# Performance work log

Hardware: AMD Instinct MI355X
Metric: run time of the kernel (lower is better)

Reference implementation:

```python
import jax, jax.numpy as jnp
import numpy as np

LARGE = 1.0e6  # sentinel distance for 'no feature pixel found'
ALPHA, GAMMA = 0.25, 2.0
SMOOTH, LAMBDA = 1e-06, 1.0


def _col_dist(feat):
    # feat: [B,H,W] bool. Distance along axis 1 to nearest True at-or-before each row.
    H = feat.shape[1]
    i = jnp.arange(H, dtype=jnp.float32)[None, :, None]
    pos = jnp.where(feat, i, -LARGE)
    return i - jax.lax.cummax(pos, axis=1)


def _edt(feat):
    # Exact Euclidean distance transform: distance from every pixel to nearest True pixel.
    # Pass 1: 1-D distance along axis 1 (two directional scans via cummax).
    g = jnp.minimum(_col_dist(feat), jnp.flip(_col_dist(jnp.flip(feat, 1)), 1))
    g = jnp.minimum(g, LARGE)  # columns with no feature
    # Pass 2: d^2(i,j) = min_k g(i,k)^2 + (j-k)^2  (exact separable EDT)
    W = feat.shape[2]
    j = jnp.arange(W, dtype=jnp.float32)
    cost = (j[:, None] - j[None, :]) ** 2  # [W(j), W(k)]
    d2 = jnp.min(g[:, :, None, :] ** 2 + cost[None, None, :, :], axis=-1)  # [B,H,W]
    return jnp.sqrt(d2)


def _distance_weights(targets_f):
    # targets_f: [B,1,H,W] float 0/1 -> beta weights [B,1,H,W]
    m = targets_f[:, 0]  # [B,H,W]
    fg = _edt(m <= 0.5)  # dist of fg pixels to nearest bg (0 on bg) == scipy edt(m>0.5)
    bg = _edt(m > 0.5)   # dist of bg pixels to nearest fg (0 on fg) == scipy edt(m<=0.5)
    dist = jnp.where(m > 0.5, fg, -bg)
    max_dist = jnp.maximum(fg.max((1, 2)), bg.max((1, 2)))  # [B]
    has_fg = m.max((1, 2)) > 0
    valid = jnp.logical_and(has_fg, max_dist > 0)
    safe_md = jnp.maximum(max_dist, 1e-12)[:, None, None]
    w = 1.0 + jnp.exp(-jnp.abs(dist) / (safe_md / 3.0))
    w = jnp.where(valid[:, None, None], w, 1.0)
    return w[:, None]  # [B,1,H,W]


def _focal_loss(logits, t):
    p = jax.nn.sigmoid(logits)
    ce = -(t * jax.nn.log_sigmoid(logits) + (1.0 - t) * jax.nn.log_sigmoid(-logits))
    p_t = p * t + (1.0 - p) * (1.0 - t)
    focal_w = (1.0 - p_t) ** GAMMA
    alpha_t = ALPHA * t + (1.0 - ALPHA) * (1.0 - t)
    return jnp.mean(alpha_t * focal_w * ce)


def _iou_loss(logits, t, w):
    p = jax.nn.sigmoid(logits)
    inter = jnp.sum(p * t * w, axis=(2, 3))          # [B,1]
    union = jnp.sum((p + t) * w, axis=(2, 3)) - inter
    iou = (inter + SMOOTH) / (union + SMOOTH)
    return 1.0 - jnp.mean(iou)


def setup_inputs() -> dict:
    key = jax.random.key(0)
    ks = jax.random.split(key, 5)
    B, H, W = 8, 256, 256
    shp = (B, 1, H, W)
    return {
        "pred_main": jax.random.normal(ks[0], shp, jnp.float32),
        "aux0": jax.random.normal(ks[1], shp, jnp.float32),
        "aux1": jax.random.normal(ks[2], shp, jnp.float32),
        "aux2": jax.random.normal(ks[3], shp, jnp.float32),
        "targets": jax.random.randint(ks[4], shp, 0, 2).astype(jnp.int32),
    }


def reference(pred_main, aux0, aux1, aux2, targets):
    t = targets.astype(jnp.float32)
    beta = _distance_weights(t)
    total = LAMBDA * _focal_loss(pred_main, t) + _iou_loss(pred_main, t, beta)
    for i, aux in enumerate((aux0, aux1, aux2)):
        aux_loss = LAMBDA * _focal_loss(aux, t) + _iou_loss(aux, t, beta)
        total = total + (0.4 / (i + 1)) * aux_loss
    return total
```

## Files before the change

### kernel.cpp

```cpp
#include <hip/hip_runtime.h>
#include <math.h>

#define HH 256
#define WW 256
#define BB 8
#define NTOT (BB*HH*WW)
#define LARGE_F 1000000.0f
#define SCOPE __HIP_MEMORY_SCOPE_AGENT

typedef unsigned int u32;
typedef unsigned long long u64;


__device__ __forceinline__ float wave_max(float v) {
    #pragma unroll
    for (int off = 32; off > 0; off >>= 1)
        v = fmaxf(v, __shfl_xor(v, off, 64));
    return v;
}

__device__ __forceinline__ void build_row(const int* __restrict__ tgt, int tb,
                                          int row, int lane, u64 (*sm)[4]) {
    const int base = tb + (row << 8) + lane;
    u64 w0 = __ballot(tgt[base]       == 0);
    u64 w1 = __ballot(tgt[base + 64]  == 0);
    u64 w2 = __ballot(tgt[base + 128] == 0);
    u64 w3 = __ballot(tgt[base + 192] == 0);
    if (lane == 0) { sm[row][0] = w0; sm[row][1] = w1; sm[row][2] = w2; sm[row][3] = w3; }
}

__device__ __forceinline__ void row_check(const u64* __restrict__ row,
                                          int k0, int r0, int c0, float dh2f,
                                          float* bestA, float* bestB) {
    u64 m0 = row[0], m1 = row[1], m2 = row[2], m3 = row[3];
    u64 n0 = ~m0, n1 = ~m1, n2 = ~m2, n3 = ~m3;

    int HbA = -1;
    if (k0 > 0 && m0) HbA = 63  - __builtin_clzll(m0);
    if (k0 > 1 && m1) HbA = 127 - __builtin_clzll(m1);
    if (k0 > 2 && m2) HbA = 191 - __builtin_clzll(m2);
    int RaA = 1 << 20;
    if (k0 < 3 && m3) RaA = 192 + __builtin_ctzll(m3);
    if (k0 < 2 && m2) RaA = 128 + __builtin_ctzll(m2);
    if (k0 < 1 && m1) RaA = 64  + __builtin_ctzll(m1);

    int HbB = -1;
    if (k0 > 0 && n0) HbB = 63  - __builtin_clzll(n0);
    if (k0 > 1 && n1) HbB = 127 - __builtin_clzll(n1);
    if (k0 > 2 && n2) HbB = 191 - __builtin_clzll(n2);
    int RaB = 1 << 20;
    if (k0 < 3 && n3) RaB = 192 + __builtin_ctzll(n3);
    if (k0 < 2 && n2) RaB = 128 + __builtin_ctzll(n2);
    if (k0 < 1 && n1) RaB = 64  + __builtin_ctzll(n1);

    u64 mk = (k0 == 0) ? m0 : (k0 == 1) ? m1 : (k0 == 2) ? m2 : m3;
    u64 nk = ~mk;
    const int base = 64 * k0;

    #pragma unroll
    for (int s = 0; s < 4; ++s) {
        int r = r0 + s, w = c0 + s;
        u64 le = (2ull << r) - 1ull;
        u64 ge = (~0ull) << r;
        {
            u64 lo = mk & le, hi = mk & ge;
            int L = lo ? (base + 63 - __builtin_clzll(lo)) : HbA;
            int R = hi ? (base + __builtin_ctzll(hi)) : RaA;
            int dl = (L >= 0) ? (w - L) : (1 << 20);
            int dr = R - w;
            float f = (float)min(dl, dr);
            bestA[s] = fminf(bestA[s], __builtin_fmaf(f, f, dh2f));
        }
        {
            u64 lo = nk & le, hi = nk & ge;
            int L = lo ? (base + 63 - __builtin_clzll(lo)) : HbB;
            int R = hi ? (base + __builtin_ctzll(hi)) : RaB;
            int dl = (L >= 0) ? (w - L) : (1 << 20);
            int dr = R - w;
            float f = (float)min(dl, dr);
            bestB[s] = fminf(bestB[s], __builtin_fmaf(f, f, dh2f));
        }
    }
}

__global__ void __launch_bounds__(512) k_fused(
    const float* __restrict__ p0, const float* __restrict__ p1,
    const float* __restrict__ p2, const float* __restrict__ p3,
    const int* __restrict__ tgt,
    u64* __restrict__ slabAB, float* __restrict__ partial,
    float* __restrict__ out)
{
    const int blk  = blockIdx.x;
    const int b    = blk >> 5;
    const int slab = blk & 31;
    const int wv   = threadIdx.x >> 6;
    const int lane = threadIdx.x & 63;
    const int h    = slab * 8 + wv;
    const int c0   = lane * 4;
    const int k0   = c0 >> 6;
    const int r0   = c0 & 63;
    const int tb   = b << 16;
    const int rowbase = tb + (h << 8);

    __shared__ u64 sm[HH][4];
    __shared__ float wredA[8], wredB[8], smdv[2];
    __shared__ float red[8][12];
    __shared__ float fing[96];

    const int lo0 = slab * 8 - 8;
    #pragma unroll
    for (int j = 0; j < 3; ++j) {
        int row = lo0 + wv * 3 + j;
        if (row >= 0 && row < HH) build_row(tgt, tb, row, lane, sm);
    }

    const int idx = rowbase + c0;
    float4 x40 = *(const float4*)(p0 + idx);
    float4 x41 = *(const float4*)(p1 + idx);
    float4 x42 = *(const float4*)(p2 + idx);
    float4 x43 = *(const float4*)(p3 + idx);

    __syncthreads();
    int winLo = max(lo0, 0);
    int winHi = min(lo0 + 23, HH - 1);

    float bestA[4] = {1e30f, 1e30f, 1e30f, 1e30f};
    float bestB[4] = {1e30f, 1e30f, 1e30f, 1e30f};

    row_check(&sm[h][0], k0, r0, c0, 0.0f, bestA, bestB);
    float bmax = 0.0f;
    #pragma unroll
    for (int s = 0; s < 4; ++s) bmax = fmaxf(bmax, fmaxf(bestA[s], bestB[s]));
    float wbmax = wave_max(bmax);

    for (int dh = 1; dh < HH; ++dh) {
        float dh2f = (float)(dh * dh);
        if (dh2f >= wbmax) break;
        int hd = h - dh, hu = h + dh;
        if (hd >= 0) {
            if (hd < winLo) { build_row(tgt, tb, hd, lane, sm); winLo = hd; }
            row_check(&sm[hd][0], k0, r0, c0, dh2f, bestA, bestB);
        }
        if (hu < HH) {
            if (hu > winHi) { build_row(tgt, tb, hu, lane, sm); winHi = hu; }
            row_check(&sm[hu][0], k0, r0, c0, dh2f, bestA, bestB);
        }
        bmax = 0.0f;
        #pragma unroll
        for (int s = 0; s < 4; ++s) bmax = fmaxf(bmax, fmaxf(bestA[s], bestB[s]));
        wbmax = wave_max(bmax);
    }

    const bool emptyB = (bestB[0] >= 1e29f);
    const u64 mkown = sm[h][k0];
    float absd[4], tfv[4];
    float wmA = -1.0f, wmB = -1.0f;
    #pragma unroll
    for (int s = 0; s < 4; ++s) {
        float dA = (bestA[s] >= 1e29f) ? LARGE_F : sqrtf(bestA[s]);
        float dB = (bestB[s] >= 1e29f) ? LARGE_F : sqrtf(bestB[s]);
        wmA = fmaxf(wmA, dA);
        wmB = fmaxf(wmB, dB);
        int bit = (int)((mkown >> (r0 + s)) & 1ull);
        tfv[s]  = bit ? 0.0f : 1.0f;
        absd[s] = bit ? dB : dA;
    }
    #pragma unroll
    for (int off = 32; off > 0; off >>= 1) {
        wmA = fmaxf(wmA, __shfl_down(wmA, off, 64));
        wmB = fmaxf(wmB, __shfl_down(wmB, off, 64));
    }
    if (lane == 0) { wredA[wv] = wmA; wredB[wv] = wmB; }
    __syncthreads();
    if (threadIdx.x == 0) {
        float bA = wredA[0], bB = wredB[0];
        #pragma unroll
        for (int j = 1; j < 8; ++j) {
            bA = fmaxf(bA, wredA[j]);
            bB = fmaxf(bB, wredB[j]);
        }
        u64 pk = ((u64)__float_as_uint(bB) << 32) | (u64)__float_as_uint(bA);
        __hip_atomic_store(&slabAB[blk], pk, __ATOMIC_RELAXED, SCOPE);
    }

    float vals[12];
    #pragma unroll
    for (int q = 0; q < 12; ++q) vals[q] = 0.0f;
    float pv[4][4];
    #pragma unroll
    for (int s = 0; s < 4; ++s) {
        float tf = tfv[s];
        #pragma unroll
        for (int i = 0; i < 4; ++i) {
            float x = (s == 0) ? ((i==0)?x40.x:(i==1)?x41.x:(i==2)?x42.x:x43.x)
                    : (s == 1) ? ((i==0)?x40.y:(i==1)?x41.y:(i==2)?x42.y:x43.y)
                    : (s == 2) ? ((i==0)?x40.z:(i==1)?x41.z:(i==2)?x42.z:x43.z)
                               : ((i==0)?x40.w:(i==1)?x41.w:(i==2)?x42.w:x43.w);
            float e = __expf(-x);
            float p = __builtin_amdgcn_rcpf(1.0f + e);
            float emabs = (x >= 0.0f) ? e : __builtin_amdgcn_rcpf(e);
            float ls = fminf(x, 0.0f) - __logf(1.0f + emabs);
            float ce = (1.0f - tf) * x - ls;
            float p_t = p * tf + (1.0f - p) * (1.0f - tf);
            float om = 1.0f - p_t;
            float alpha_t = 0.25f * tf + 0.75f * (1.0f - tf);
            vals[i] += alpha_t * om * om * ce;
            pv[s][i] = p;
        }
    }

    if (wv == 0) {
        float a = 0.0f, bb = 0.0f;
        if (lane < 32) {
            const int i = (b << 5) + lane;
            u64 v;
            for (;;) {
                v = __hip_atomic_load(&slabAB[i], __ATOMIC_RELAXED, SCOPE);
                if (!(v & 0x8000000080000000ull)) break;
                __builtin_amdgcn_s_sleep(1);
            }
            a  = __uint_as_float((u32)v);
            bb = __uint_as_float((u32)(v >> 32));
        }
        #pragma unroll
        for (int off = 32; off > 0; off >>= 1) {
            a  = fmaxf(a,  __shfl_xor(a,  off, 64));
            bb = fmaxf(bb, __shfl_xor(bb, off, 64));
        }
        if (lane == 0) { smdv[0] = a; smdv[1] = bb; }
    }
    __syncthreads();
    const float md = fmaxf(smdv[0], smdv[1]);
    const bool valid = (!emptyB) && (md > 0.0f);
    const float inv = 3.0f / fmaxf(md, 1e-12f);

    #pragma unroll
    for (int s = 0; s < 4; ++s) {
        float wgt = valid ? (1.0f + __expf(-absd[s] * inv)) : 1.0f;
        float tf = tfv[s];
        #pragma unroll
        for (int i = 0; i < 4; ++i) {
            vals[4 + i] += tf * pv[s][i] * wgt;
            vals[8 + i] += (pv[s][i] + tf) * wgt;
        }
    }

    #pragma unroll
    for (int q = 0; q < 12; ++q) {
        float v = vals[q];
        #pragma unroll
        for (int o = 32; o > 0; o >>= 1) v += __shfl_down(v, o, 64);
        if (lane == 0) red[wv][q] = v;
    }
    __syncthreads();
    if (threadIdx.x < 12) {
        int q = threadIdx.x;
        float s = 0.0f;
        #pragma unroll
        for (int j = 0; j < 8; ++j) s += red[j][q];
        __hip_atomic_store((u32*)&partial[blk * 12 + q], __float_as_uint(s),
                           __ATOMIC_RELAXED, SCOPE);
    }

    if (blk == 0) {
        if (threadIdx.x < 96) {
            const int bi = threadIdx.x / 12;
            const int qq = threadIdx.x % 12;
            float acc8[8];
            #pragma unroll
            for (int j = 0; j < 8; ++j) acc8[j] = 0.0f;
            for (int g4 = 0; g4 < 4; ++g4) {
                u32 raw[8];
                for (;;) {
                    bool bad = false;
                    #pragma unroll
                    for (int j = 0; j < 8; ++j)
                        raw[j] = __hip_atomic_load((u32*)&partial[((bi << 5) + g4 * 8 + j) * 12 + qq],
                                                   __ATOMIC_RELAXED, SCOPE);
                    #pragma unroll
                    for (int j = 0; j < 8; ++j) bad = bad || ((raw[j] >> 31) != 0u);
                    if (!bad) break;
                    __builtin_amdgcn_s_sleep(1);
                }
                #pragma unroll
                for (int j = 0; j < 8; ++j) acc8[j] += __uint_as_float(raw[j]);
            }
            fing[threadIdx.x] = ((acc8[0]+acc8[1])+(acc8[2]+acc8[3]))
                              + ((acc8[4]+acc8[5])+(acc8[6]+acc8[7]));
        }
        __syncthreads();
        if (threadIdx.x == 0) {
            const float coef[4] = {1.0f, 0.4f, 0.2f, 0.4f / 3.0f};
            float total = 0.0f;
            #pragma unroll
            for (int i = 0; i < 4; ++i) {
                float fm = 0.0f, ious = 0.0f;
                #pragma unroll
                for (int b2 = 0; b2 < BB; ++b2) {
                    fm += fing[b2 * 12 + i];
                    float in_ = fing[b2 * 12 + 4 + i];
                    float un  = fing[b2 * 12 + 8 + i] - in_;
                    ious += (in_ + 1e-6f) / (un + 1e-6f);
                }
                total += coef[i] * (fm / (float)NTOT + (1.0f - ious * 0.125f));
            }
            out[0] = total;
        }
    }
}

extern "C" void kernel_launch(void* const* d_in, const int* in_sizes, int n_in,
                              void* d_out, int out_size, void* d_ws, size_t ws_size,
                              hipStream_t stream) {
    const float* p0 = (const float*)d_in[0];
    const float* p1 = (const float*)d_in[1];
    const float* p2 = (const float*)d_in[2];
    const float* p3 = (const float*)d_in[3];
    const int* tgt = (const int*)d_in[4];
    float* out = (float*)d_out;

    char* w = (char*)d_ws;
    u64* slabAB    = (u64*)w;   w += 256 * sizeof(u64);
    float* partial = (float*)w; w += 256 * 12 * sizeof(float);

    k_fused<<<BB * 32, 512, 0, stream>>>(p0, p1, p2, p3, tgt, slabAB, partial, out);
}
```

Before: 80.53 us.

## Split fused kernel into three launches, replacing spin-wait grid sync

Replaces the single fused kernel, which used atomic spin-waits on per-slab max values and partial sums, with three kernels: EDT plus focal loss, IoU weighting, and a final reduction. Signed distances go to a global scratch buffer and are read back in the second kernel, which also reloads all four prediction tensors and recomputes the sigmoid. This removes the busy-wait polling and its dependence on every block being resident at once. In exchange it adds two kernel launches and extra global memory traffic.

```diff
diff --git a/kernel.cpp b/kernel.cpp
--- a/kernel.cpp
+++ b/kernel.cpp
@@ -6,7 +6,6 @@
 #define BB 8
 #define NTOT (BB*HH*WW)
 #define LARGE_F 1000000.0f
-#define SCOPE __HIP_MEMORY_SCOPE_AGENT
 
 typedef unsigned int u32;
 typedef unsigned long long u64;
@@ -83,12 +82,12 @@
     }
 }
 
-__global__ void __launch_bounds__(512) k_fused(
+__global__ void __launch_bounds__(512) k_edt_focal(
     const float* __restrict__ p0, const float* __restrict__ p1,
     const float* __restrict__ p2, const float* __restrict__ p3,
     const int* __restrict__ tgt,
     u64* __restrict__ slabAB, float* __restrict__ partial,
-    float* __restrict__ out)
+    float* __restrict__ sdbuf)
 {
     const int blk  = blockIdx.x;
     const int b    = blk >> 5;
@@ -100,12 +99,11 @@
     const int k0   = c0 >> 6;
     const int r0   = c0 & 63;
     const int tb   = b << 16;
-    const int rowbase = tb + (h << 8);
+    const int idx  = tb + (h << 8) + c0;
 
     __shared__ u64 sm[HH][4];
-    __shared__ float wredA[8], wredB[8], smdv[2];
-    __shared__ float red[8][12];
-    __shared__ float fing[96];
+    __shared__ float wredA[8], wredB[8];
+    __shared__ float red[8][4];
 
     const int lo0 = slab * 8 - 8;
     #pragma unroll
@@ -114,7 +112,6 @@
         if (row >= 0 && row < HH) build_row(tgt, tb, row, lane, sm);
     }
 
-    const int idx = rowbase + c0;
     float4 x40 = *(const float4*)(p0 + idx);
     float4 x41 = *(const float4*)(p1 + idx);
     float4 x42 = *(const float4*)(p2 + idx);
@@ -151,9 +148,8 @@
         wbmax = wave_max(bmax);
     }
 
-    const bool emptyB = (bestB[0] >= 1e29f);
     const u64 mkown = sm[h][k0];
-    float absd[4], tfv[4];
+    float tfv[4], sdv[4];
     float wmA = -1.0f, wmB = -1.0f;
     #pragma unroll
     for (int s = 0; s < 4; ++s) {
@@ -162,31 +158,20 @@
         wmA = fmaxf(wmA, dA);
         wmB = fmaxf(wmB, dB);
         int bit = (int)((mkown >> (r0 + s)) & 1ull);
-        tfv[s]  = bit ? 0.0f : 1.0f;
-        absd[s] = bit ? dB : dA;
-    }
+        tfv[s] = bit ? 0.0f : 1.0f;
+        sdv[s] = bit ? -dB : dA;
+    }
+    float4 sd4; sd4.x = sdv[0]; sd4.y = sdv[1]; sd4.z = sdv[2]; sd4.w = sdv[3];
+    *(float4*)(sdbuf + idx) = sd4;
+
     #pragma unroll
     for (int off = 32; off > 0; off >>= 1) {
         wmA = fmaxf(wmA, __shfl_down(wmA, off, 64));
         wmB = fmaxf(wmB, __shfl_down(wmB, off, 64));
     }
     if (lane == 0) { wredA[wv] = wmA; wredB[wv] = wmB; }
-    __syncthreads();
-    if (threadIdx.x == 0) {
-        float bA = wredA[0], bB = wredB[0];
-        #pragma unroll
-        for (int j = 1; j < 8; ++j) {
-            bA = fmaxf(bA, wredA[j]);
-            bB = fmaxf(bB, wredB[j]);
-        }
-        u64 pk = ((u64)__float_as_uint(bB) << 32) | (u64)__float_as_uint(bA);
-        __hip_atomic_store(&slabAB[blk], pk, __ATOMIC_RELAXED, SCOPE);
-    }
-
-    float vals[12];
-    #pragma unroll
-    for (int q = 0; q < 12; ++q) vals[q] = 0.0f;
-    float pv[4][4];
+
+    float vals[4] = {0.0f, 0.0f, 0.0f, 0.0f};
     #pragma unroll
     for (int s = 0; s < 4; ++s) {
         float tf = tfv[s];
@@ -205,107 +190,151 @@
             float om = 1.0f - p_t;
             float alpha_t = 0.25f * tf + 0.75f * (1.0f - tf);
             vals[i] += alpha_t * om * om * ce;
-            pv[s][i] = p;
-        }
-    }
-
-    if (wv == 0) {
-        float a = 0.0f, bb = 0.0f;
-        if (lane < 32) {
-            const int i = (b << 5) + lane;
-            u64 v;
-            for (;;) {
-                v = __hip_atomic_load(&slabAB[i], __ATOMIC_RELAXED, SCOPE);
-                if (!(v & 0x8000000080000000ull)) break;
-                __builtin_amdgcn_s_sleep(1);
-            }
-            a  = __uint_as_float((u32)v);
-            bb = __uint_as_float((u32)(v >> 32));
-        }
-        #pragma unroll
-        for (int off = 32; off > 0; off >>= 1) {
-            a  = fmaxf(a,  __shfl_xor(a,  off, 64));
-            bb = fmaxf(bb, __shfl_xor(bb, off, 64));
-        }
-        if (lane == 0) { smdv[0] = a; smdv[1] = bb; }
-    }
-    __syncthreads();
-    const float md = fmaxf(smdv[0], smdv[1]);
-    const bool valid = (!emptyB) && (md > 0.0f);
-    const float inv = 3.0f / fmaxf(md, 1e-12f);
-
-    #pragma unroll
-    for (int s = 0; s < 4; ++s) {
-        float wgt = valid ? (1.0f + __expf(-absd[s] * inv)) : 1.0f;
-        float tf = tfv[s];
-        #pragma unroll
-        for (int i = 0; i < 4; ++i) {
-            vals[4 + i] += tf * pv[s][i] * wgt;
-            vals[8 + i] += (pv[s][i] + tf) * wgt;
-        }
-    }
-
-    #pragma unroll
-    for (int q = 0; q < 12; ++q) {
+        }
+    }
+    #pragma unroll
+    for (int q = 0; q < 4; ++q) {
         float v = vals[q];
         #pragma unroll
         for (int o = 32; o > 0; o >>= 1) v += __shfl_down(v, o, 64);
         if (lane == 0) red[wv][q] = v;
     }
     __syncthreads();
-    if (threadIdx.x < 12) {
+    if (threadIdx.x == 0) {
+        float bA = wredA[0], bB = wredB[0];
+        #pragma unroll
+        for (int j = 1; j < 8; ++j) {
+            bA = fmaxf(bA, wredA[j]);
+            bB = fmaxf(bB, wredB[j]);
+        }
+        slabAB[blk] = ((u64)__float_as_uint(bB) << 32) | (u64)__float_as_uint(bA);
+    }
+    if (threadIdx.x < 4) {
         int q = threadIdx.x;
         float s = 0.0f;
         #pragma unroll
         for (int j = 0; j < 8; ++j) s += red[j][q];
-        __hip_atomic_store((u32*)&partial[blk * 12 + q], __float_as_uint(s),
-                           __ATOMIC_RELAXED, SCOPE);
-    }
-
-    if (blk == 0) {
-        if (threadIdx.x < 96) {
-            const int bi = threadIdx.x / 12;
-            const int qq = threadIdx.x % 12;
-            float acc8[8];
+        partial[blk * 12 + q] = s;
+    }
+}
+
+__global__ void __launch_bounds__(512) k_iou(
+    const float* __restrict__ p0, const float* __restrict__ p1,
+    const float* __restrict__ p2, const float* __restrict__ p3,
+    const u64* __restrict__ slabAB, float* __restrict__ partial,
+    const float* __restrict__ sdbuf)
+{
+    const int blk  = blockIdx.x;
+    const int b    = blk >> 5;
+    const int slab = blk & 31;
+    const int wv   = threadIdx.x >> 6;
+    const int lane = threadIdx.x & 63;
+    const int h    = slab * 8 + wv;
+    const int c0   = lane * 4;
+    const int idx  = (b << 16) + (h << 8) + c0;
+
+    __shared__ float smdv[2];
+    __shared__ float red[8][8];
+
+    if (threadIdx.x < 32) {
+        u64 v = slabAB[(b << 5) + threadIdx.x];
+        float a  = __uint_as_float((u32)v);
+        float bb = __uint_as_float((u32)(v >> 32));
+        #pragma unroll
+        for (int off = 16; off > 0; off >>= 1) {
+            a  = fmaxf(a,  __shfl_xor(a,  off, 32));
+            bb = fmaxf(bb, __shfl_xor(bb, off, 32));
+        }
+        if (threadIdx.x == 0) { smdv[0] = a; smdv[1] = bb; }
+    }
+
+    float4 x40 = *(const float4*)(p0 + idx);
+    float4 x41 = *(const float4*)(p1 + idx);
+    float4 x42 = *(const float4*)(p2 + idx);
+    float4 x43 = *(const float4*)(p3 + idx);
+    float4 sd4 = *(const float4*)(sdbuf + idx);
+
+    __syncthreads();
+    const float wB = smdv[1];
+    const float md = fmaxf(smdv[0], wB);
+    const bool valid = (wB != LARGE_F) && (md > 0.0f);
+    const float inv = 3.0f / fmaxf(md, 1e-12f);
+
+    float vals[8];
+    #pragma unroll
+    for (int q = 0; q < 8; ++q) vals[q] = 0.0f;
+
+    #pragma unroll
+    for (int s = 0; s < 4; ++s) {
+        float sd = (s == 0) ? sd4.x : (s == 1) ? sd4.y : (s == 2) ? sd4.z : sd4.w;
+        float tf = (sd > 0.0f) ? 1.0f : 0.0f;
+        float absd = fabsf(sd);
+        float wgt = valid ? (1.0f + __expf(-absd * inv)) : 1.0f;
+        #pragma unroll
+        for (int i = 0; i < 4; ++i) {
+            float x = (s == 0) ? ((i==0)?x40.x:(i==1)?x41.x:(i==2)?x42.x:x43.x)
+                    : (s == 1) ? ((i==0)?x40.y:(i==1)?x41.y:(i==2)?x42.y:x43.y)
+                    : (s == 2) ? ((i==0)?x40.z:(i==1)?x41.z:(i==2)?x42.z:x43.z)
+                               : ((i==0)?x40.w:(i==1)?x41.w:(i==2)?x42.w:x43.w);
+            float e = __expf(-x);
+            float p = __builtin_amdgcn_rcpf(1.0f + e);
+            vals[i]     += tf * p * wgt;
+            vals[4 + i] += (p + tf) * wgt;
+        }
+    }
+
+    #pragma unroll
+    for (int q = 0; q < 8; ++q) {
+        float v = vals[q];
+        #pragma unroll
+        for (int o = 32; o > 0; o >>= 1) v += __shfl_down(v, o, 64);
+        if (lane == 0) red[wv][q] = v;
+    }
+    __syncthreads();
+    if (threadIdx.x < 8) {
+        int q = threadIdx.x;
+        float s = 0.0f;
+        #pragma unroll
+        for (int j = 0; j < 8; ++j) s += red[j][q];
+        partial[blk * 12 + 4 + q] = s;
+    }
+}
+
+__global__ void k_final(const float* __restrict__ partial, float* __restrict__ out)
+{
+    __shared__ float fing[96];
+    if (threadIdx.x < 96) {
+        const int bi = threadIdx.x / 12;
+        const int qq = threadIdx.x % 12;
+        float acc8[8];
+        #pragma unroll
+        for (int j = 0; j < 8; ++j) acc8[j] = 0.0f;
+        #pragma unroll
+        for (int g4 = 0; g4 < 4; ++g4) {
             #pragma unroll
-            for (int j = 0; j < 8; ++j) acc8[j] = 0.0f;
-            for (int g4 = 0; g4 < 4; ++g4) {
-                u32 raw[8];
-                for (;;) {
-                    bool bad = false;
-                    #pragma unroll
-                    for (int j = 0; j < 8; ++j)
-                        raw[j] = __hip_atomic_load((u32*)&partial[((bi << 5) + g4 * 8 + j) * 12 + qq],
-                                                   __ATOMIC_RELAXED, SCOPE);
-                    #pragma unroll
-                    for (int j = 0; j < 8; ++j) bad = bad || ((raw[j] >> 31) != 0u);
-                    if (!bad) break;
-                    __builtin_amdgcn_s_sleep(1);
-                }
-                #pragma unroll
-                for (int j = 0; j < 8; ++j) acc8[j] += __uint_as_float(raw[j]);
+            for (int j = 0; j < 8; ++j)
+                acc8[j] += partial[((bi << 5) + g4 * 8 + j) * 12 + qq];
+        }
+        fing[threadIdx.x] = ((acc8[0]+acc8[1])+(acc8[2]+acc8[3]))
+                          + ((acc8[4]+acc8[5])+(acc8[6]+acc8[7]));
+    }
+    __syncthreads();
+    if (threadIdx.x == 0) {
+        const float coef[4] = {1.0f, 0.4f, 0.2f, 0.4f / 3.0f};
+        float total = 0.0f;
+        #pragma unroll
+        for (int i = 0; i < 4; ++i) {
+            float fm = 0.0f, ious = 0.0f;
+            #pragma unroll
+            for (int b2 = 0; b2 < BB; ++b2) {
+                fm += fing[b2 * 12 + i];
+                float in_ = fing[b2 * 12 + 4 + i];
+                float un  = fing[b2 * 12 + 8 + i] - in_;
+                ious += (in_ + 1e-6f) / (un + 1e-6f);
             }
-            fing[threadIdx.x] = ((acc8[0]+acc8[1])+(acc8[2]+acc8[3]))
-                              + ((acc8[4]+acc8[5])+(acc8[6]+acc8[7]));
-        }
-        __syncthreads();
-        if (threadIdx.x == 0) {
-            const float coef[4] = {1.0f, 0.4f, 0.2f, 0.4f / 3.0f};
-            float total = 0.0f;
-            #pragma unroll
-            for (int i = 0; i < 4; ++i) {
-                float fm = 0.0f, ious = 0.0f;
-                #pragma unroll
-                for (int b2 = 0; b2 < BB; ++b2) {
-                    fm += fing[b2 * 12 + i];
-                    float in_ = fing[b2 * 12 + 4 + i];
-                    float un  = fing[b2 * 12 + 8 + i] - in_;
-                    ious += (in_ + 1e-6f) / (un + 1e-6f);
-                }
-                total += coef[i] * (fm / (float)NTOT + (1.0f - ious * 0.125f));
-            }
-            out[0] = total;
-        }
+            total += coef[i] * (fm / (float)NTOT + (1.0f - ious * 0.125f));
+        }
+        out[0] = total;
     }
 }
 
@@ -322,6 +351,11 @@
     char* w = (char*)d_ws;
     u64* slabAB    = (u64*)w;   w += 256 * sizeof(u64);
     float* partial = (float*)w; w += 256 * 12 * sizeof(float);
-
-    k_fused<<<BB * 32, 512, 0, stream>>>(p0, p1, p2, p3, tgt, slabAB, partial, out);
-}
+    float* sdbuf   = (float*)w;
+
+    k_edt_focal<<<BB * 32, 512, 0, stream>>>(p0, p1, p2, p3, tgt,
+                                             slabAB, partial, sdbuf);
+    k_iou<<<BB * 32, 512, 0, stream>>>(p0, p1, p2, p3,
+                                       slabAB, partial, sdbuf);
+    k_final<<<1, 128, 0, stream>>>(partial, out);
+}
```

New measurement: 82.58 us. 1.03x slower.
